# Optimization experiments

Hardware: AMD Instinct MI355X
Metric: run time of the kernel (lower is better)

## Reference

```python
import jax, jax.numpy as jnp
import numpy as np

N_NODES = 100000
N_EDGES = 1600000
EPS = 1e-5
ALPHA = 0.01  # leaky relu slope


def gcn_conv(x, src, dst, W, b, n_nodes):
    """PyG GCNConv: h = W x, add self-loops, out = D^-1/2 (A+I) D^-1/2 h + b."""
    h = x @ W  # [N, d_out]
    # add self loops
    loop = jnp.arange(n_nodes, dtype=src.dtype)
    s = jnp.concatenate([src, loop])
    d = jnp.concatenate([dst, loop])
    # symmetric normalization: deg computed at destination over A + I
    deg = jax.ops.segment_sum(jnp.ones_like(d, dtype=h.dtype), d, num_segments=n_nodes)
    dinv = jnp.where(deg > 0, jax.lax.rsqrt(deg), 0.0)
    norm = dinv[s] * dinv[d]  # [E+N]
    msg = h[s] * norm[:, None]  # gather + scale (memory bound)
    out = jax.ops.segment_sum(msg, d, num_segments=n_nodes)
    return out + b


def batch_norm(x, gamma, beta):
    mu = jnp.mean(x, axis=0)
    var = jnp.var(x, axis=0)
    return (x - mu) * jax.lax.rsqrt(var + EPS) * gamma + beta


def setup_inputs() -> dict:
    key = jax.random.key(0)
    ks = jax.random.split(key, 6)
    emb = jax.random.normal(ks[0], (N_NODES, 64), dtype=jnp.float32)
    edge_index = jax.random.randint(ks[1], (2, N_EDGES), 0, N_NODES, dtype=jnp.int32)
    W1 = jax.random.normal(ks[2], (64, 128), dtype=jnp.float32) * 0.05
    W2 = jax.random.normal(ks[3], (128, 256), dtype=jnp.float32) * 0.05
    Wf = jax.random.normal(ks[4], (256, 256), dtype=jnp.float32) * 0.05
    return {
        "embeddings": emb, "edge_index": edge_index,
        "W1": W1, "b1": jnp.zeros((128,), jnp.float32),
        "g1": jnp.ones((128,), jnp.float32), "beta1": jnp.zeros((128,), jnp.float32),
        "W2": W2, "b2": jnp.zeros((256,), jnp.float32),
        "g2": jnp.ones((256,), jnp.float32), "beta2": jnp.zeros((256,), jnp.float32),
        "Wf": Wf, "bf": jnp.zeros((256,), jnp.float32),
    }


def reference(embeddings, edge_index, W1, b1, g1, beta1, W2, b2, g2, beta2, Wf, bf):
    src, dst = edge_index[0], edge_index[1]
    x = gcn_conv(embeddings, src, dst, W1, b1, N_NODES)
    x = batch_norm(x, g1, beta1)
    x = jnp.where(x >= 0, x, ALPHA * x)  # leaky relu; dropout = identity (eval)
    x = gcn_conv(x, src, dst, W2, b2, N_NODES)
    x = batch_norm(x, g2, beta2)
    x = jnp.where(x >= 0, x, ALPHA * x)
    return x @ Wf + bf
```

## Files before the change

kernel.cpp:

```cpp
#include <hip/hip_runtime.h>

#define NN 100000
#define NE 1600000
constexpr float EPS_BN = 1e-5f;
constexpr float ALPHA = 0.01f;
constexpr int GBN = 128;
constexpr int NBUCK = (NN + 127) / 128;
constexpr int GA = 128;
constexpr int EPB = NE / GA;

typedef __attribute__((ext_vector_type(8))) short short8;
typedef __attribute__((ext_vector_type(4))) float f32x4;

__device__ __forceinline__ float bfu2f(uint lo16) {
    union { uint i; float f; } v; v.i = lo16 << 16; return v.f;
}
__device__ __forceinline__ float bfhi2f(uint u) {
    union { uint i; float f; } v; v.i = u & 0xffff0000u; return v.f;
}
__device__ __forceinline__ ushort f2bf(float f) {
    union { float f; uint i; } v; v.f = f;
    return (ushort)((v.i + 0x7fffu + ((v.i >> 16) & 1u)) >> 16);
}

__global__ __launch_bounds__(256) void k_bhist(const int* __restrict__ dstv, int* __restrict__ bcnt) {
    __shared__ int hist[NBUCK];
    for (int i = threadIdx.x; i < NBUCK; i += 256) hist[i] = 0;
    __syncthreads();
    int base = blockIdx.x * EPB;
    for (int i = threadIdx.x; i < EPB; i += 256)
        atomicAdd(&hist[dstv[base + i] >> 7], 1);
    __syncthreads();
    for (int i = threadIdx.x; i < NBUCK; i += 256)
        bcnt[blockIdx.x * NBUCK + i] = hist[i];
}

__global__ __launch_bounds__(1024) void k_bscan(const int* __restrict__ bcnt,
                                                int* __restrict__ gcur, int* __restrict__ bbase) {
    __shared__ int tot[1024];
    int b = threadIdx.x;
    int t = 0;
    if (b < NBUCK)
        for (int k = 0; k < GA; ++k) t += bcnt[k * NBUCK + b];
    tot[b] = t;
    __syncthreads();
    for (int off = 1; off < 1024; off <<= 1) {
        int u = (b >= off) ? tot[b - off] : 0;
        __syncthreads();
        tot[b] += u;
        __syncthreads();
    }
    int ex = tot[b] - t;
    if (b < NBUCK) {
        bbase[b] = ex;
        int cur = ex;
        for (int k = 0; k < GA; ++k) { gcur[k * NBUCK + b] = cur; cur += bcnt[k * NBUCK + b]; }
    }
    if (b == 0) bbase[NBUCK] = NE;
}

__global__ __launch_bounds__(256) void k_bscatter(const int* __restrict__ srcv, const int* __restrict__ dstv,
                                                  const int* __restrict__ gcur, uint* __restrict__ bpair) {
    __shared__ int lcur[NBUCK];
    for (int i = threadIdx.x; i < NBUCK; i += 256) lcur[i] = gcur[blockIdx.x * NBUCK + i];
    __syncthreads();
    int base = blockIdx.x * EPB;
    for (int i = threadIdx.x; i < EPB; i += 256) {
        int d = dstv[base + i], s = srcv[base + i];
        int slot = atomicAdd(&lcur[d >> 7], 1);
        bpair[slot] = ((uint)(d & 127) << 17) | (uint)s;
    }
}

__global__ __launch_bounds__(256) void k_bcsr(const uint* __restrict__ bpair, const int* __restrict__ bbase,
                                              int* __restrict__ col, int* __restrict__ cnt,
                                              int* __restrict__ indptr, float* __restrict__ dinv) {
    __shared__ int h[128];
    __shared__ int off[128];
    int b = blockIdx.x, t = threadIdx.x;
    int p0 = bbase[b], p1 = bbase[b + 1];
    if (t < 128) h[t] = 0;
    __syncthreads();
    for (int i = p0 + t; i < p1; i += 256)
        atomicAdd(&h[bpair[i] >> 17], 1);
    __syncthreads();
    if (t < 128) off[t] = h[t];
    __syncthreads();
    for (int o = 1; o < 128; o <<= 1) {
        int u = 0;
        if (t < 128 && t >= o) u = off[t - o];
        __syncthreads();
        if (t < 128) off[t] += u;
        __syncthreads();
    }
    if (t < 128) {
        int st = p0 + off[t] - h[t];
        int node = b * 128 + t;
        if (node < NN) {
            indptr[node] = st;
            cnt[node] = h[t];
            dinv[node] = rsqrtf((float)(h[t] + 1));
        }
        off[t] = st;
    }
    __syncthreads();
    for (int i = p0 + t; i < p1; i += 256) {
        uint u = bpair[i];
        int slot = atomicAdd(&off[u >> 17], 1);
        col[slot] = (int)(u & 0x1FFFFu);
    }
}

__global__ void k_wtrans_all(const float* __restrict__ W1, const float* __restrict__ W2,
                             const float* __restrict__ Wf, ushort* __restrict__ w1t,
                             ushort* __restrict__ w2t, ushort* __restrict__ wft) {
    int i = blockIdx.x * 256 + threadIdx.x;
    if (i < 8192) {
        int m = i / 64, k = i % 64;
        w1t[i] = f2bf(W1[(size_t)k * 128 + m]);
    } else if (i < 8192 + 32768) {
        int j = i - 8192;
        int m = j / 128, k = j % 128;
        w2t[j] = f2bf(W2[(size_t)k * 256 + m]);
    } else if (i < 8192 + 32768 + 65536) {
        int j = i - 8192 - 32768;
        int m = j / 256, k = j % 256;
        wft[j] = f2bf(Wf[(size_t)k * 256 + m]);
    }
}

__global__ __launch_bounds__(256) void k_semb(const float* __restrict__ emb, const float* __restrict__ dinv,
                                              uint2* __restrict__ embs) {
    int i = blockIdx.x * 256 + threadIdx.x;
    if (i >= NN * 16) return;
    int row = i >> 4;
    float dn = dinv[row];
    float4 f = ((const float4*)emb)[i];
    uint2 o;
    o.x = (uint)f2bf(f.x * dn) | ((uint)f2bf(f.y * dn) << 16);
    o.y = (uint)f2bf(f.z * dn) | ((uint)f2bf(f.w * dn) << 16);
    embs[i] = o;
}

__global__ __launch_bounds__(256) void k_x2s(const ushort* __restrict__ H1, const float* __restrict__ sc,
                                             const float* __restrict__ sh, const float* __restrict__ dinv,
                                             ushort* __restrict__ x2s) {
    int i = blockIdx.x * 256 + threadIdx.x;
    if (i >= NN * 16) return;
    int row = i >> 4, f0 = (i & 15) * 8;
    float dn = dinv[row];
    uint4 u = ((const uint4*)H1)[i];
    uint uu[4] = {u.x, u.y, u.z, u.w};
    uint oo[4];
#pragma unroll
    for (int q = 0; q < 4; ++q) {
        int f = f0 + q * 2;
        float e0 = bfu2f(uu[q] & 0xffffu) * sc[f] + sh[f];
        float e1 = bfhi2f(uu[q]) * sc[f + 1] + sh[f + 1];
        e0 = ((e0 >= 0.f) ? e0 : ALPHA * e0) * dn;
        e1 = ((e1 >= 0.f) ? e1 : ALPHA * e1) * dn;
        oo[q] = (uint)f2bf(e0) | ((uint)f2bf(e1) << 16);
    }
    uint4 o; o.x = oo[0]; o.y = oo[1]; o.z = oo[2]; o.w = oo[3];
    ((uint4*)x2s)[i] = o;
}

template <int W>
__global__ __launch_bounds__(64) void k_agg(const ushort* __restrict__ X, const int* __restrict__ indptr,
                                            const int* __restrict__ cnt, const int* __restrict__ col,
                                            const float* __restrict__ dinv, ushort* __restrict__ out) {
    int n = blockIdx.x, t = threadIdx.x;
    __shared__ int sc[64];
    int start = indptr[n], c = cnt[n];
    if constexpr (W == 64) {
        float a0 = bfu2f(X[(size_t)n * 64 + t]);
        for (int base = 0; base < c; base += 64) {
            int m = min(64, c - base);
            if (t < m) sc[t] = col[start + base + t];
            __syncthreads();
#pragma unroll 4
            for (int j = 0; j < m; ++j)
                a0 += bfu2f(X[(size_t)sc[j] * 64 + t]);
            __syncthreads();
        }
        out[(size_t)n * 64 + t] = f2bf(a0 * dinv[n]);
    } else {
        const uint* Xu = (const uint*)X;
        uint u = Xu[(size_t)n * 64 + t];
        float a0 = bfu2f(u & 0xffffu), a1 = bfhi2f(u);
        for (int base = 0; base < c; base += 64) {
            int m = min(64, c - base);
            if (t < m) sc[t] = col[start + base + t];
            __syncthreads();
#pragma unroll 4
            for (int j = 0; j < m; ++j) {
                uint v = Xu[(size_t)sc[j] * 64 + t];
                a0 += bfu2f(v & 0xffffu); a1 += bfhi2f(v);
            }
            __syncthreads();
        }
        float dn = dinv[n];
        ((uint*)out)[(size_t)n * 64 + t] = (uint)f2bf(a0 * dn) | ((uint)f2bf(a1 * dn) << 16);
    }
}

template <int K, int NOUT, int AT, int OUT>
__global__ __launch_bounds__(256) void k_mgemm(
        const void* __restrict__ Ap, const ushort* __restrict__ BT, void* __restrict__ Cp,
        const float* __restrict__ scale, const float* __restrict__ shift,
        const float* __restrict__ bias) {
    constexpr int BM = 128, BK = 32, LDA = 40;
    constexpr int WN = NOUT / 2;
    constexpr int NF = WN / 16;
    __shared__ ushort As[BM * LDA];
    __shared__ ushort Bs[NOUT * LDA];
    __shared__ float s_sc[K];
    __shared__ float s_sh[K];

    int tid = threadIdx.x;
    int brow = blockIdx.x * BM;
    if constexpr (AT == 1) {
        for (int i = tid; i < K; i += 256) { s_sc[i] = scale[i]; s_sh[i] = shift[i]; }
        __syncthreads();
    }

    int lane = tid & 63, wid = tid >> 6;
    int wr = wid >> 1, wc = wid & 1;
    int fr = lane & 15, fq = lane >> 4;
    int fk = fq * 8;

    f32x4 acc[4][NF];
#pragma unroll
    for (int mi = 0; mi < 4; ++mi)
#pragma unroll
        for (int ni = 0; ni < NF; ++ni) acc[mi][ni] = (f32x4){0.f, 0.f, 0.f, 0.f};

    const int srow = tid >> 1, sk0 = (tid & 1) * 16;
    const int grow = brow + srow;
    const bool aok = grow < NN;

    for (int kk = 0; kk < K; kk += BK) {
        __align__(16) ushort tmp[16];
#pragma unroll
        for (int j = 0; j < 16; ++j) tmp[j] = 0;
        if (aok) {
            const ushort* ap = (const ushort*)Ap + (size_t)grow * K + kk + sk0;
            if constexpr (AT == 2) {
                *(uint4*)&tmp[0] = *(const uint4*)ap;
                *(uint4*)&tmp[8] = *(const uint4*)(ap + 8);
            } else {
                uint4 u0 = *(const uint4*)ap;
                uint4 u1 = *(const uint4*)(ap + 8);
                uint uu[8] = {u0.x, u0.y, u0.z, u0.w, u1.x, u1.y, u1.z, u1.w};
#pragma unroll
                for (int q = 0; q < 8; ++q) {
                    int kq = kk + sk0 + q * 2;
                    float e0 = bfu2f(uu[q] & 0xffffu) * s_sc[kq] + s_sh[kq];
                    float e1 = bfhi2f(uu[q]) * s_sc[kq + 1] + s_sh[kq + 1];
                    e0 = (e0 >= 0.f) ? e0 : ALPHA * e0;
                    e1 = (e1 >= 0.f) ? e1 : ALPHA * e1;
                    tmp[q * 2 + 0] = f2bf(e0);
                    tmp[q * 2 + 1] = f2bf(e1);
                }
            }
        }
        *(uint4*)&As[srow * LDA + sk0] = *(uint4*)&tmp[0];
        *(uint4*)&As[srow * LDA + sk0 + 8] = *(uint4*)&tmp[8];

#pragma unroll
        for (int it = 0; it < NOUT * BK / (256 * 8); ++it) {
            int idx = tid + it * 256;
            int bro = idx >> 2, bk = (idx & 3) * 8;
            *(uint4*)&Bs[bro * LDA + bk] = *(const uint4*)(BT + (size_t)bro * K + kk + bk);
        }

        __syncthreads();

        short8 af[4], bfv[NF];
#pragma unroll
        for (int mi = 0; mi < 4; ++mi)
            af[mi] = *(const short8*)&As[(wr * 64 + mi * 16 + fr) * LDA + fk];
#pragma unroll
        for (int ni = 0; ni < NF; ++ni)
            bfv[ni] = *(const short8*)&Bs[(wc * WN + ni * 16 + fr) * LDA + fk];
#pragma unroll
        for (int mi = 0; mi < 4; ++mi)
#pragma unroll
            for (int ni = 0; ni < NF; ++ni)
                acc[mi][ni] = __builtin_amdgcn_mfma_f32_16x16x32_bf16(af[mi], bfv[ni], acc[mi][ni], 0, 0, 0);

        __syncthreads();
    }

    float bv[NF];
#pragma unroll
    for (int ni = 0; ni < NF; ++ni) bv[ni] = bias[wc * WN + ni * 16 + fr];

    if constexpr (OUT == 1) {
        float* outf = (float*)Cp;
#pragma unroll
        for (int mi = 0; mi < 4; ++mi)
#pragma unroll
            for (int r = 0; r < 4; ++r) {
                int row = brow + wr * 64 + mi * 16 + fq * 4 + r;
                if (row < NN) {
#pragma unroll
                    for (int ni = 0; ni < NF; ++ni) {
                        int c = wc * WN + ni * 16 + fr;
                        outf[(size_t)row * NOUT + c] = acc[mi][ni][r] + bv[ni];
                    }
                }
            }
    } else {
        ushort* outb = (ushort*)Cp;
#pragma unroll
        for (int mi = 0; mi < 4; ++mi)
#pragma unroll
            for (int r = 0; r < 4; ++r) {
                int row = brow + wr * 64 + mi * 16 + fq * 4 + r;
                if (row < NN) {
#pragma unroll
                    for (int ni = 0; ni < NF; ++ni) {
                        int c = wc * WN + ni * 16 + fr;
                        outb[(size_t)row * NOUT + c] = f2bf(acc[mi][ni][r] + bv[ni]);
                    }
                }
            }
    }
}

template <int M>
__global__ __launch_bounds__(256) void k_bnpart(const ushort* __restrict__ X, float* __restrict__ partials) {
    constexpr int FG = M / 8, RP = 256 / FG;
    __shared__ float rs[RP * M];
    __shared__ float rq[RP * M];
    int fg = threadIdx.x % FG, r0 = threadIdx.x / FG;
    float s[8] = {0, 0, 0, 0, 0, 0, 0, 0}, q[8] = {0, 0, 0, 0, 0, 0, 0, 0};
    for (int n = blockIdx.x * RP + r0; n < NN; n += GBN * RP) {
        uint4 u = ((const uint4*)X)[(size_t)n * FG + fg];
        uint uu[4] = {u.x, u.y, u.z, u.w};
#pragma unroll
        for (int p = 0; p < 4; ++p) {
            float v0 = bfu2f(uu[p] & 0xffffu), v1 = bfhi2f(uu[p]);
            s[p * 2] += v0; q[p * 2] += v0 * v0;
            s[p * 2 + 1] += v1; q[p * 2 + 1] += v1 * v1;
        }
    }
    int f0 = fg * 8;
#pragma unroll
    for (int j = 0; j < 8; ++j) {
        rs[r0 * M + f0 + j] = s[j];
        rq[r0 * M + f0 + j] = q[j];
    }
    __syncthreads();
    for (int h = RP / 2; h; h >>= 1) {
        if (r0 < h) {
#pragma unroll
            for (int j = 0; j < 8; ++j) {
                rs[r0 * M + f0 + j] += rs[(r0 + h) * M + f0 + j];
                rq[r0 * M + f0 + j] += rq[(r0 + h) * M + f0 + j];
            }
        }
        __syncthreads();
    }
    if (threadIdx.x < M) {
        partials[(size_t)blockIdx.x * 2 * M + threadIdx.x] = rs[threadIdx.x];
        partials[(size_t)blockIdx.x * 2 * M + M + threadIdx.x] = rq[threadIdx.x];
    }
}

template <int M>
__global__ void k_bnred(const float* __restrict__ partials, const float* __restrict__ g,
                        const float* __restrict__ be, float* __restrict__ scale,
                        float* __restrict__ shift) {
    int f = threadIdx.x;
    if (f < M) {
        float s = 0.f, q = 0.f;
        for (int b = 0; b < GBN; ++b) {
            s += partials[(size_t)b * 2 * M + f];
            q += partials[(size_t)b * 2 * M + M + f];
        }
        float mu = s * (1.f / NN);
        float var = q * (1.f / NN) - mu * mu;
        float r = rsqrtf(var + EPS_BN);
        float sc = g[f] * r;
        scale[f] = sc;
        shift[f] = be[f] - mu * sc;
    }
}

extern "C" void kernel_launch(void* const* d_in, const int* in_sizes, int n_in,
                              void* d_out, int out_size, void* d_ws, size_t ws_size,
                              hipStream_t stream) {
    const float* emb = (const float*)d_in[0];
    const int* eidx  = (const int*)d_in[1];
    const float* W1  = (const float*)d_in[2];
    const float* b1  = (const float*)d_in[3];
    const float* g1  = (const float*)d_in[4];
    const float* be1 = (const float*)d_in[5];
    const float* W2  = (const float*)d_in[6];
    const float* b2  = (const float*)d_in[7];
    const float* g2  = (const float*)d_in[8];
    const float* be2 = (const float*)d_in[9];
    const float* Wf  = (const float*)d_in[10];
    const float* bf  = (const float*)d_in[11];
    float* out = (float*)d_out;
    const int* srcv = eidx;
    const int* dstv = eidx + NE;

    char* w = (char*)d_ws;
    auto alloc = [&](size_t bytes) {
        char* p = w;
        w += (bytes + 255) / 256 * 256;
        return p;
    };
    int* cnt    = (int*)alloc((size_t)NN * 4);
    int* indptr = (int*)alloc((size_t)NN * 4);
    int* bcnt   = (int*)alloc((size_t)NBUCK * GA * 4);
    int* gcur   = (int*)alloc((size_t)NBUCK * GA * 4);
    int* bbase  = (int*)alloc((size_t)(NBUCK + 1) * 4);
    int* colb   = (int*)alloc((size_t)NE * 4);
    uint* bpair = (uint*)alloc((size_t)NE * 4);
    float* dinv = (float*)alloc((size_t)NN * 4);
    float* partials = (float*)alloc((size_t)GBN * 512 * 4);
    float* sc1 = (float*)alloc(128 * 4);
    float* sh1 = (float*)alloc(128 * 4);
    float* sc2 = (float*)alloc(256 * 4);
    float* sh2 = (float*)alloc(256 * 4);
    ushort* w1t = (ushort*)alloc((size_t)128 * 64 * 2);
    ushort* w2t = (ushort*)alloc((size_t)256 * 128 * 2);
    ushort* wft = (ushort*)alloc((size_t)256 * 256 * 2);
    ushort* slabA = (ushort*)alloc((size_t)NN * 128 * 2);
    ushort* slabB = (ushort*)alloc((size_t)NN * 128 * 2);
    ushort* H2 = (ushort*)alloc((size_t)NN * 256 * 2);

    ushort* embs = slabA;
    ushort* aggE = slabB;
    ushort* H1   = slabA;
    ushort* x2s  = slabB;
    ushort* agg2 = slabA;

    k_bhist<<<GA, 256, 0, stream>>>(dstv, bcnt);
    k_bscan<<<1, 1024, 0, stream>>>(bcnt, gcur, bbase);
    k_bscatter<<<GA, 256, 0, stream>>>(srcv, dstv, gcur, bpair);
    k_bcsr<<<NBUCK, 256, 0, stream>>>(bpair, bbase, colb, cnt, indptr, dinv);

    k_wtrans_all<<<(8192 + 32768 + 65536 + 255) / 256, 256, 0, stream>>>(W1, W2, Wf, w1t, w2t, wft);

    constexpr int GX = (NN + 127) / 128;

    k_semb<<<(NN * 16 + 255) / 256, 256, 0, stream>>>(emb, dinv, (uint2*)embs);
    k_agg<64><<<NN, 64, 0, stream>>>(embs, indptr, cnt, colb, dinv, aggE);
    k_mgemm<64, 128, 2, 2><<<GX, 256, 0, stream>>>(aggE, w1t, H1, nullptr, nullptr, b1);
    k_bnpart<128><<<GBN, 256, 0, stream>>>(H1, partials);
    k_bnred<128><<<1, 256, 0, stream>>>(partials, g1, be1, sc1, sh1);

    k_x2s<<<(NN * 16 + 255) / 256, 256, 0, stream>>>(H1, sc1, sh1, dinv, x2s);
    k_agg<128><<<NN, 64, 0, stream>>>(x2s, indptr, cnt, colb, dinv, agg2);
    k_mgemm<128, 256, 2, 2><<<GX, 256, 0, stream>>>(agg2, w2t, H2, nullptr, nullptr, b2);
    k_bnpart<256><<<GBN, 256, 0, stream>>>(H2, partials);
    k_bnred<256><<<1, 256, 0, stream>>>(partials, g2, be2, sc2, sh2);

    k_mgemm<256, 256, 1, 1><<<GX, 256, 0, stream>>>(H2, wft, out, sc2, sh2, bf);
}
```

Before: 382.2 us.

## Split gather lanes in aggregation, double-buffer A tile and read B from global in GEMM

The 64-wide aggregation now has each half-wavefront process alternate neighbours with 32-bit loads, then combines the halves with a cross-lane shuffle. The 128-wide aggregation uses two independent accumulators so more loads are in flight. The GEMM changes to 64-row tiles with each of the four waves owning a column slice. It double-buffers the A tile in shared memory with prefetch and one barrier per k-step, and loads B fragments directly from global memory instead of staging them in LDS. This aims to cut barrier stalls and raise memory-level parallelism. The costs are more redundant global traffic for B and smaller tiles.

Result: faster. 364.3 us (-4.7%).

```diff
diff --git a/kernel.cpp b/kernel.cpp
--- a/kernel.cpp
+++ b/kernel.cpp
@@ -165,42 +165,88 @@
     ((uint4*)x2s)[i] = o;
 }
 
-template <int W>
-__global__ __launch_bounds__(64) void k_agg(const ushort* __restrict__ X, const int* __restrict__ indptr,
-                                            const int* __restrict__ cnt, const int* __restrict__ col,
-                                            const float* __restrict__ dinv, ushort* __restrict__ out) {
+__global__ __launch_bounds__(64) void k_agg64(const ushort* __restrict__ X, const int* __restrict__ indptr,
+                                              const int* __restrict__ cnt, const int* __restrict__ col,
+                                              const float* __restrict__ dinv, ushort* __restrict__ out) {
+    int n = blockIdx.x, t = threadIdx.x;
+    int t2 = t & 31, h = t >> 5;
+    __shared__ int sc[64];
+    int start = indptr[n], c = cnt[n];
+    const uint* Xu = (const uint*)X;
+    float a0 = 0.f, a1 = 0.f;
+    if (h == 0) {
+        uint u = Xu[(size_t)n * 32 + t2];
+        a0 = bfu2f(u & 0xffffu); a1 = bfhi2f(u);
+    }
+    for (int base = 0; base < c; base += 64) {
+        int m = min(64, c - base);
+        if (t < m) sc[t] = col[start + base + t];
+        __syncthreads();
+#pragma unroll 2
+        for (int j = h; j < m; j += 2) {
+            uint v = Xu[(size_t)sc[j] * 32 + t2];
+            a0 += bfu2f(v & 0xffffu); a1 += bfhi2f(v);
+        }
+        __syncthreads();
+    }
+    a0 += __shfl_xor(a0, 32);
+    a1 += __shfl_xor(a1, 32);
+    if (h == 0) {
+        float dn = dinv[n];
+        ((uint*)out)[(size_t)n * 32 + t2] = (uint)f2bf(a0 * dn) | ((uint)f2bf(a1 * dn) << 16);
+    }
+}
+
+__global__ __launch_bounds__(64) void k_agg128(const ushort* __restrict__ X, const int* __restrict__ indptr,
+                                               const int* __restrict__ cnt, const int* __restrict__ col,
+                                               const float* __restrict__ dinv, ushort* __restrict__ out) {
     int n = blockIdx.x, t = threadIdx.x;
     __shared__ int sc[64];
     int start = indptr[n], c = cnt[n];
-    if constexpr (W == 64) {
-        float a0 = bfu2f(X[(size_t)n * 64 + t]);
-        for (int base = 0; base < c; base += 64) {
-            int m = min(64, c - base);
-            if (t < m) sc[t] = col[start + base + t];
-            __syncthreads();
-#pragma unroll 4
-            for (int j = 0; j < m; ++j)
-                a0 += bfu2f(X[(size_t)sc[j] * 64 + t]);
-            __syncthreads();
-        }
-        out[(size_t)n * 64 + t] = f2bf(a0 * dinv[n]);
+    const uint* Xu = (const uint*)X;
+    uint u = Xu[(size_t)n * 64 + t];
+    float a0 = bfu2f(u & 0xffffu), a1 = bfhi2f(u);
+    float b0 = 0.f, b1 = 0.f;
+    for (int base = 0; base < c; base += 64) {
+        int m = min(64, c - base);
+        if (t < m) sc[t] = col[start + base + t];
+        __syncthreads();
+        int j = 0;
+#pragma unroll 2
+        for (; j + 2 <= m; j += 2) {
+            uint v0 = Xu[(size_t)sc[j] * 64 + t];
+            uint v1 = Xu[(size_t)sc[j + 1] * 64 + t];
+            a0 += bfu2f(v0 & 0xffffu); a1 += bfhi2f(v0);
+            b0 += bfu2f(v1 & 0xffffu); b1 += bfhi2f(v1);
+        }
+        if (j < m) {
+            uint v = Xu[(size_t)sc[j] * 64 + t];
+            a0 += bfu2f(v & 0xffffu); a1 += bfhi2f(v);
+        }
+        __syncthreads();
+    }
+    a0 += b0; a1 += b1;
+    float dn = dinv[n];
+    ((uint*)out)[(size_t)n * 64 + t] = (uint)f2bf(a0 * dn) | ((uint)f2bf(a1 * dn) << 16);
+}
+
+template <int AT>
+__device__ __forceinline__ uint4 xform8(uint4 u, int kbase, const float* s_sc, const float* s_sh) {
+    if constexpr (AT == 1) {
+        uint uu[4] = {u.x, u.y, u.z, u.w};
+        uint oo[4];
+#pragma unroll
+        for (int q = 0; q < 4; ++q) {
+            int kq = kbase + q * 2;
+            float e0 = bfu2f(uu[q] & 0xffffu) * s_sc[kq] + s_sh[kq];
+            float e1 = bfhi2f(uu[q]) * s_sc[kq + 1] + s_sh[kq + 1];
+            e0 = (e0 >= 0.f) ? e0 : ALPHA * e0;
+            e1 = (e1 >= 0.f) ? e1 : ALPHA * e1;
+            oo[q] = (uint)f2bf(e0) | ((uint)f2bf(e1) << 16);
+        }
+        return make_uint4(oo[0], oo[1], oo[2], oo[3]);
     } else {
-        const uint* Xu = (const uint*)X;
-        uint u = Xu[(size_t)n * 64 + t];
-        float a0 = bfu2f(u & 0xffffu), a1 = bfhi2f(u);
-        for (int base = 0; base < c; base += 64) {
-            int m = min(64, c - base);
-            if (t < m) sc[t] = col[start + base + t];
-            __syncthreads();
-#pragma unroll 4
-            for (int j = 0; j < m; ++j) {
-                uint v = Xu[(size_t)sc[j] * 64 + t];
-                a0 += bfu2f(v & 0xffffu); a1 += bfhi2f(v);
-            }
-            __syncthreads();
-        }
-        float dn = dinv[n];
-        ((uint*)out)[(size_t)n * 64 + t] = (uint)f2bf(a0 * dn) | ((uint)f2bf(a1 * dn) << 16);
+        return u;
     }
 }
 
@@ -209,92 +255,72 @@
         const void* __restrict__ Ap, const ushort* __restrict__ BT, void* __restrict__ Cp,
         const float* __restrict__ scale, const float* __restrict__ shift,
         const float* __restrict__ bias) {
-    constexpr int BM = 128, BK = 32, LDA = 40;
-    constexpr int WN = NOUT / 2;
+    constexpr int BM = 64, BK = 32, LDA = 40;
+    constexpr int WN = NOUT / 4;
     constexpr int NF = WN / 16;
-    __shared__ ushort As[BM * LDA];
-    __shared__ ushort Bs[NOUT * LDA];
+    constexpr int NT = K / BK;
+    __shared__ ushort As[2][BM * LDA];
     __shared__ float s_sc[K];
     __shared__ float s_sh[K];
 
     int tid = threadIdx.x;
     int brow = blockIdx.x * BM;
+    int lane = tid & 63, wid = tid >> 6;
+    int fr = lane & 15, fq = lane >> 4;
+    int fk = fq * 8;
+
+    const int srow = tid >> 2, sk0 = (tid & 3) * 8;
+    const int grow = brow + srow;
+    const bool aok = grow < NN;
+    const ushort* arp = (const ushort*)Ap + (size_t)grow * K + sk0;
+
     if constexpr (AT == 1) {
         for (int i = tid; i < K; i += 256) { s_sc[i] = scale[i]; s_sh[i] = shift[i]; }
         __syncthreads();
     }
 
-    int lane = tid & 63, wid = tid >> 6;
-    int wr = wid >> 1, wc = wid & 1;
-    int fr = lane & 15, fq = lane >> 4;
-    int fk = fq * 8;
-
     f32x4 acc[4][NF];
 #pragma unroll
     for (int mi = 0; mi < 4; ++mi)
 #pragma unroll
         for (int ni = 0; ni < NF; ++ni) acc[mi][ni] = (f32x4){0.f, 0.f, 0.f, 0.f};
 
-    const int srow = tid >> 1, sk0 = (tid & 1) * 16;
-    const int grow = brow + srow;
-    const bool aok = grow < NN;
-
-    for (int kk = 0; kk < K; kk += BK) {
-        __align__(16) ushort tmp[16];
-#pragma unroll
-        for (int j = 0; j < 16; ++j) tmp[j] = 0;
-        if (aok) {
-            const ushort* ap = (const ushort*)Ap + (size_t)grow * K + kk + sk0;
-            if constexpr (AT == 2) {
-                *(uint4*)&tmp[0] = *(const uint4*)ap;
-                *(uint4*)&tmp[8] = *(const uint4*)(ap + 8);
-            } else {
-                uint4 u0 = *(const uint4*)ap;
-                uint4 u1 = *(const uint4*)(ap + 8);
-                uint uu[8] = {u0.x, u0.y, u0.z, u0.w, u1.x, u1.y, u1.z, u1.w};
-#pragma unroll
-                for (int q = 0; q < 8; ++q) {
-                    int kq = kk + sk0 + q * 2;
-                    float e0 = bfu2f(uu[q] & 0xffffu) * s_sc[kq] + s_sh[kq];
-                    float e1 = bfhi2f(uu[q]) * s_sc[kq + 1] + s_sh[kq + 1];
-                    e0 = (e0 >= 0.f) ? e0 : ALPHA * e0;
-                    e1 = (e1 >= 0.f) ? e1 : ALPHA * e1;
-                    tmp[q * 2 + 0] = f2bf(e0);
-                    tmp[q * 2 + 1] = f2bf(e1);
-                }
-            }
-        }
-        *(uint4*)&As[srow * LDA + sk0] = *(uint4*)&tmp[0];
-        *(uint4*)&As[srow * LDA + sk0 + 8] = *(uint4*)&tmp[8];
-
-#pragma unroll
-        for (int it = 0; it < NOUT * BK / (256 * 8); ++it) {
-            int idx = tid + it * 256;
-            int bro = idx >> 2, bk = (idx & 3) * 8;
-            *(uint4*)&Bs[bro * LDA + bk] = *(const uint4*)(BT + (size_t)bro * K + kk + bk);
-        }
-
-        __syncthreads();
-
-        short8 af[4], bfv[NF];
+    uint4 av = make_uint4(0, 0, 0, 0);
+    if (aok) av = *(const uint4*)arp;
+    av = xform8<AT>(av, sk0, s_sc, s_sh);
+    *(uint4*)&As[0][srow * LDA + sk0] = av;
+
+    for (int t = 0; t < NT; ++t) {
+        __syncthreads();
+        uint4 anext = make_uint4(0, 0, 0, 0);
+        if (t + 1 < NT && aok)
+            anext = *(const uint4*)(arp + (t + 1) * BK);
+
+        short8 bfv[NF];
+#pragma unroll
+        for (int ni = 0; ni < NF; ++ni)
+            bfv[ni] = *(const short8*)(BT + (size_t)(wid * WN + ni * 16 + fr) * K + t * BK + fk);
+
+        short8 af[4];
 #pragma unroll
         for (int mi = 0; mi < 4; ++mi)
-            af[mi] = *(const short8*)&As[(wr * 64 + mi * 16 + fr) * LDA + fk];
-#pragma unroll
-        for (int ni = 0; ni < NF; ++ni)
-            bfv[ni] = *(const short8*)&Bs[(wc * WN + ni * 16 + fr) * LDA + fk];
+            af[mi] = *(const short8*)&As[t & 1][(mi * 16 + fr) * LDA + fk];
+
 #pragma unroll
         for (int mi = 0; mi < 4; ++mi)
 #pragma unroll
             for (int ni = 0; ni < NF; ++ni)
                 acc[mi][ni] = __builtin_amdgcn_mfma_f32_16x16x32_bf16(af[mi], bfv[ni], acc[mi][ni], 0, 0, 0);
 
-        __syncthreads();
+        if (t + 1 < NT) {
+            anext = xform8<AT>(anext, (t + 1) * BK + sk0, s_sc, s_sh);
+            *(uint4*)&As[(t + 1) & 1][srow * LDA + sk0] = anext;
+        }
     }
 
     float bv[NF];
 #pragma unroll
-    for (int ni = 0; ni < NF; ++ni) bv[ni] = bias[wc * WN + ni * 16 + fr];
+    for (int ni = 0; ni < NF; ++ni) bv[ni] = bias[wid * WN + ni * 16 + fr];
 
     if constexpr (OUT == 1) {
         float* outf = (float*)Cp;
@@ -302,11 +328,11 @@
         for (int mi = 0; mi < 4; ++mi)
 #pragma unroll
             for (int r = 0; r < 4; ++r) {
-                int row = brow + wr * 64 + mi * 16 + fq * 4 + r;
+                int row = brow + mi * 16 + fq * 4 + r;
                 if (row < NN) {
 #pragma unroll
                     for (int ni = 0; ni < NF; ++ni) {
-                        int c = wc * WN + ni * 16 + fr;
+                        int c = wid * WN + ni * 16 + fr;
                         outf[(size_t)row * NOUT + c] = acc[mi][ni][r] + bv[ni];
                     }
                 }
@@ -317,11 +343,11 @@
         for (int mi = 0; mi < 4; ++mi)
 #pragma unroll
             for (int r = 0; r < 4; ++r) {
-                int row = brow + wr * 64 + mi * 16 + fq * 4 + r;
+                int row = brow + mi * 16 + fq * 4 + r;
                 if (row < NN) {
 #pragma unroll
                     for (int ni = 0; ni < NF; ++ni) {
-                        int c = wc * WN + ni * 16 + fr;
+                        int c = wid * WN + ni * 16 + fr;
                         outb[(size_t)row * NOUT + c] = f2bf(acc[mi][ni][r] + bv[ni]);
                     }
                 }
@@ -447,16 +473,16 @@
 
     k_wtrans_all<<<(8192 + 32768 + 65536 + 255) / 256, 256, 0, stream>>>(W1, W2, Wf, w1t, w2t, wft);
 
-    constexpr int GX = (NN + 127) / 128;
+    constexpr int GX = (NN + 63) / 64;
 
     k_semb<<<(NN * 16 + 255) / 256, 256, 0, stream>>>(emb, dinv, (uint2*)embs);
-    k_agg<64><<<NN, 64, 0, stream>>>(embs, indptr, cnt, colb, dinv, aggE);
+    k_agg64<<<NN, 64, 0, stream>>>(embs, indptr, cnt, colb, dinv, aggE);
     k_mgemm<64, 128, 2, 2><<<GX, 256, 0, stream>>>(aggE, w1t, H1, nullptr, nullptr, b1);
     k_bnpart<128><<<GBN, 256, 0, stream>>>(H1, partials);
     k_bnred<128><<<1, 256, 0, stream>>>(partials, g1, be1, sc1, sh1);
 
     k_x2s<<<(NN * 16 + 255) / 256, 256, 0, stream>>>(H1, sc1, sh1, dinv, x2s);
-    k_agg<128><<<NN, 64, 0, stream>>>(x2s, indptr, cnt, colb, dinv, agg2);
+    k_agg128<<<NN, 64, 0, stream>>>(x2s, indptr, cnt, colb, dinv, agg2);
     k_mgemm<128, 256, 2, 2><<<GX, 256, 0, stream>>>(agg2, w2t, H2, nullptr, nullptr, b2);
     k_bnpart<256><<<GBN, 256, 0, stream>>>(H2, partials);
     k_bnred<256><<<1, 256, 0, stream>>>(partials, g2, be2, sc2, sh2);
```
